# Performance work log

Measured on AMD Instinct MI355X. Metric: run time of the kernel, lower is better.

The kernel has to match this reference:

```python
import jax, jax.numpy as jnp
import numpy as np

B, T, G, D = 32, 120, 25, 256
H, HD = 8, 32  # H*HD == D
EPS = 1e-6


def _xavier(key, out_f, in_f):
    lim = float(np.sqrt(6.0 / (in_f + out_f)))
    return jax.random.uniform(key, (out_f, in_f), jnp.float32, -lim, lim)


def setup_inputs() -> dict:
    key = jax.random.key(0)
    ks = jax.random.split(key, 12)
    inp = {
        "x": jax.random.normal(ks[0], (B, T, G, D), jnp.float32),
        "adjacency_matrix": jax.random.uniform(ks[1], (G, G), jnp.float32),
        "Wq": _xavier(ks[2], H * HD, D), "bq": jnp.zeros((H * HD,), jnp.float32),
        "Wk": _xavier(ks[3], H * HD, D), "bk": jnp.zeros((H * HD,), jnp.float32),
        "Wv": _xavier(ks[4], H * HD, D), "bv": jnp.zeros((H * HD,), jnp.float32),
        "Wo": _xavier(ks[5], D, D), "bo": jnp.zeros((D,), jnp.float32),
        "Wfc": _xavier(ks[6], D, D), "bfc": jnp.zeros((D,), jnp.float32),
        "alpha": jnp.ones((D,), jnp.float32),
        "beta": jnp.zeros((D,), jnp.float32),
    }
    return inp


def _norm(z, alpha, beta):
    # torch: alpha * (x - mean) / (std(unbiased) + eps) + bias
    mu = jnp.mean(z, axis=-1, keepdims=True)
    sd = jnp.std(z, axis=-1, keepdims=True, ddof=1)
    return alpha * (z - mu) / (sd + EPS) + beta


def reference(x, adjacency_matrix, Wq, bq, Wk, bk, Wv, bv, Wo, bo, Wfc, bfc, alpha, beta):
    # adjacency aggregation: [G,G] @ [B,T,G,D] -> [B,T,G,D]
    h = jnp.einsum('gn,btnd->btgd', adjacency_matrix, x)

    def proj(W, b):
        # [B,T,G,D] -> [B,T,G,H,HD] -> transpose(1,2) -> [B,G,T,H,HD]
        p = (h @ W.T + b).reshape(B, T, G, H, HD)
        return jnp.swapaxes(p, 1, 2)

    Q, K, V = proj(Wq, bq), proj(Wk, bk), proj(Wv, bv)
    # scores over last two axes (H x H) -- faithful to the source's transpose quirk
    scores = (Q @ jnp.swapaxes(K, -2, -1)) / jnp.sqrt(jnp.float32(HD))  # [B,G,T,H,H]
    # F.softmax with no dim on a 5-D tensor -> torch softmaxes along dim=1 (G axis)
    w = jax.nn.softmax(scores, axis=1)
    att = w @ V  # [B,G,T,H,HD]
    att = jnp.swapaxes(att, 1, 2).reshape(B, T, G, D)
    x_att = att @ Wo.T + bo

    x1 = _norm(x + x_att, alpha, beta)
    x_fc = jax.nn.relu(x1 @ Wfc.T + bfc)
    return _norm(x1 + x_fc, alpha, beta)
```

## Files before the change

### kernel.cpp

```cpp
#include <hip/hip_runtime.h>

#define NB 32
#define NT 120
#define NG 25
#define ND 256
#define NH 8
#define NHD 32
#define NTH 512

typedef unsigned short u16;
typedef unsigned int u32;

typedef __bf16 bf16x8 __attribute__((ext_vector_type(8)));
typedef float  f32x4  __attribute__((ext_vector_type(4)));

#define SB 264
#define SF 268
#define OFF_HS_HI 0
#define OFF_HS_LO 16896
#define OFF_QKV   33792
#define OFF_ADJ   136704
#define OFF_SS    139312
#define OFF_WRED  145712
#define OFF_MU    146544
#define OFF_RSD   146656
#define SMEM_TOT  146768

#define WS_QKV_HI 0
#define WS_QKV_LO 196608
#define WS_WO_HI  393216
#define WS_WO_LO  458752
#define WS_WFC_HI 524288
#define WS_WFC_LO 589824
#define WS_NEED_BYTES (655360ull * 2ull)

__device__ __forceinline__ float bf2f(u16 u) { return __uint_as_float(((u32)u) << 16); }
__device__ __forceinline__ u16 f2bf(float f) {
    u32 x = __float_as_uint(f);
    return (u16)((x + 0x7FFFu + ((x >> 16) & 1u)) >> 16);
}
__device__ __forceinline__ void splitf(float v, u16& h, u16& l) {
    h = f2bf(v);
    l = f2bf(v - bf2f(h));
}
__device__ __forceinline__ bf16x8 ld_bf8(const u16* p) {
    uint4 u = *(const uint4*)p;
    return __builtin_bit_cast(bf16x8, u);
}

__global__ __launch_bounds__(256)
void prep_w(const float* __restrict__ Wq, const float* __restrict__ Wk,
            const float* __restrict__ Wv, const float* __restrict__ Wo,
            const float* __restrict__ Wfc, u16* __restrict__ ws) {
    int e = blockIdx.x * 256 + threadIdx.x;
    float v; int hi_base, lo_base, idx;
    if (e < 196608) {
        int n = e >> 8, k = e & 255;
        const float* W = (n < 256) ? Wq : (n < 512 ? Wk : Wv);
        v = W[(n & 255) * 256 + k];
        hi_base = WS_QKV_HI; lo_base = WS_QKV_LO; idx = e;
    } else if (e < 262144) {
        idx = e - 196608; v = Wo[idx];
        hi_base = WS_WO_HI; lo_base = WS_WO_LO;
    } else {
        idx = e - 262144; v = Wfc[idx];
        hi_base = WS_WFC_HI; lo_base = WS_WFC_LO;
    }
    u16 h, l; splitf(v, h, l);
    ws[hi_base + idx] = h;
    ws[lo_base + idx] = l;
}

__device__ __forceinline__ void norm_stats8(const float* zv, int gn,
                                            int lane, int wid, int tid,
                                            float (*s_wred)[13][2], float* s_mu, float* s_rsd) {
    #pragma unroll
    for (int i = 0; i < 13; ++i) {
        if (i >= gn) break;
        float s = zv[i], q = zv[i] * zv[i];
        #pragma unroll
        for (int off = 32; off > 0; off >>= 1) {
            s += __shfl_xor(s, off, 64);
            q += __shfl_xor(q, off, 64);
        }
        if (lane == 0) { s_wred[wid][i][0] = s; s_wred[wid][i][1] = q; }
    }
    __syncthreads();
    if (tid < NG) {
        const int g = tid;
        const int wb = (g < 13) ? 0 : 4, lg = (g < 13) ? g : g - 13;
        float s = 0.f, q = 0.f;
        #pragma unroll
        for (int w = 0; w < 4; ++w) { s += s_wred[wb + w][lg][0]; q += s_wred[wb + w][lg][1]; }
        float mu = s * (1.f / 256.f);
        float var = fmaxf((q - 256.f * mu * mu) * (1.f / 255.f), 0.f);
        s_mu[g] = mu;
        s_rsd[g] = 1.f / (sqrtf(var) + 1e-6f);
    }
    __syncthreads();
}

template<bool PREP>
__device__ __forceinline__ void load_bfrag(const u16* wshi, const u16* wslo,
                                           const float* Wf, int row, int koff,
                                           bf16x8& bh, bf16x8& bl) {
    if constexpr (PREP) {
        const int off = row * 256 + koff;
        bh = ld_bf8(wshi + off);
        bl = ld_bf8(wslo + off);
    } else {
        const float* p = Wf + row * 256 + koff;
        float4 w0 = *(const float4*)p, w1 = *(const float4*)(p + 4);
        float wv[8] = {w0.x, w0.y, w0.z, w0.w, w1.x, w1.y, w1.z, w1.w};
        union { u16 s[8]; bf16x8 v; } H, L;
        #pragma unroll
        for (int j = 0; j < 8; ++j) splitf(wv[j], H.s[j], L.s[j]);
        bh = H.v; bl = L.v;
    }
}

template<bool PREP>
__global__ __launch_bounds__(NTH, 2)
void enc_mfma(const float* __restrict__ x,  const float* __restrict__ adj,
              const float* __restrict__ Wq, const float* __restrict__ bq,
              const float* __restrict__ Wk, const float* __restrict__ bk,
              const float* __restrict__ Wv, const float* __restrict__ bv,
              const float* __restrict__ Wo, const float* __restrict__ bo,
              const float* __restrict__ Wfc,const float* __restrict__ bfc,
              const float* __restrict__ alpha, const float* __restrict__ beta,
              float* __restrict__ out, const u16* __restrict__ ws)
{
    extern __shared__ char smem[];
    u16*   hs_hi = (u16*)(smem + OFF_HS_HI);
    u16*   hs_lo = (u16*)(smem + OFF_HS_LO);
    float* qkvf  = (float*)(smem + OFF_QKV);
    float* adjf  = (float*)(smem + OFF_ADJ);
    float* ss    = (float*)(smem + OFF_SS);
    float (*s_wred)[13][2] = (float(*)[13][2])(smem + OFF_WRED);
    float* s_mu  = (float*)(smem + OFF_MU);
    float* s_rsd = (float*)(smem + OFF_RSD);

    const int bt = blockIdx.x;
    const int tid = threadIdx.x;
    const int d = tid & 255, rep = tid >> 8;
    const int lane = tid & 63, wid = tid >> 6;
    const int lm = lane & 15, quad = lane >> 4;
    const int g0 = rep ? 13 : 0, gn = rep ? 12 : 13;
    const long base = (long)bt * (NG * ND);

    auto loadA = [&](int k0, bf16x8 (&ah)[2], bf16x8 (&al)[2]) {
        const int koff = k0 + quad * 8;
        #pragma unroll
        for (int mt = 0; mt < 2; ++mt) {
            const int off = (mt * 16 + lm) * SB + koff;
            ah[mt] = ld_bf8(hs_hi + off);
            al[mt] = ld_bf8(hs_lo + off);
        }
    };
    auto loadB_qkv = [&](int k0, bf16x8 (&bh)[6], bf16x8 (&bl)[6]) {
        const int koff = k0 + quad * 8;
        #pragma unroll
        for (int j = 0; j < 6; ++j) {
            const int n0 = wid * 96 + j * 16;
            const int mat = n0 >> 8;
            const float* Wf = (mat == 0) ? Wq : (mat == 1 ? Wk : Wv);
            load_bfrag<PREP>(ws + WS_QKV_HI, ws + WS_QKV_LO, Wf,
                             PREP ? (n0 + lm) : ((n0 & 255) + lm), koff, bh[j], bl[j]);
        }
    };
    auto loadB_wo = [&](int k0, bf16x8 (&bh)[2], bf16x8 (&bl)[2]) {
        const int koff = k0 + quad * 8;
        #pragma unroll
        for (int j = 0; j < 2; ++j)
            load_bfrag<PREP>(ws + WS_WO_HI, ws + WS_WO_LO, Wo,
                             wid * 32 + j * 16 + lm, koff, bh[j], bl[j]);
    };
    auto loadB_wfc = [&](int k0, bf16x8 (&bh)[2], bf16x8 (&bl)[2]) {
        const int koff = k0 + quad * 8;
        #pragma unroll
        for (int j = 0; j < 2; ++j)
            load_bfrag<PREP>(ws + WS_WFC_HI, ws + WS_WFC_LO, Wfc,
                             wid * 32 + j * 16 + lm, koff, bh[j], bl[j]);
    };

    bf16x8 bh2[2][6], bl2[2][6];
    bf16x8 bh6[2][2], bl6[2][2];
    bf16x8 bh8[2][2], bl8[2][2];
    float zx[13];
    float zv[13];

    for (int i = tid; i < NG * NG; i += NTH) adjf[i] = adj[i];
    const float af = alpha[d], bef = beta[d];
    __syncthreads();

    {
        float acc[13];
        #pragma unroll
        for (int i = 0; i < 13; ++i) acc[i] = 0.f;
        #pragma unroll
        for (int n = 0; n < NG; ++n) {
            float xv = x[base + n * ND + d];
            if (rep == 0) { if (n < 13) zx[n] = xv; }
            else          { if (n >= 13) zx[n - 13] = xv; }
            #pragma unroll
            for (int i = 0; i < 13; ++i)
                acc[i] += adjf[(g0 + i) * NG + n] * xv;
        }
        #pragma unroll
        for (int i = 0; i < 13; ++i) {
            if (i >= gn) break;
            u16 h, l; splitf(acc[i], h, l);
            hs_hi[(g0 + i) * SB + d] = h; hs_lo[(g0 + i) * SB + d] = l;
        }
        if (rep) {
            #pragma unroll
            for (int g = NG; g < 32; ++g) { hs_hi[g * SB + d] = 0; hs_lo[g * SB + d] = 0; }
        }
    }
    loadB_qkv(0, bh2[0], bl2[0]);
    __syncthreads();

    {
        float bb[6];
        #pragma unroll
        for (int nt = 0; nt < 6; ++nt) {
            const int n0 = wid * 96 + nt * 16;
            const int mat = n0 >> 8, cb = (n0 & 255) + lm;
            const float* bp = (mat == 0) ? bq : (mat == 1 ? bk : bv);
            bb[nt] = bp[cb];
        }
        f32x4 acc[2][6];
        #pragma unroll
        for (int mt = 0; mt < 2; ++mt)
            #pragma unroll
            for (int nt = 0; nt < 6; ++nt) acc[mt][nt] = (f32x4)0.f;

        bf16x8 ah[2][2], al[2][2];
        loadA(0, ah[0], al[0]);
        #pragma unroll
        for (int ki = 0; ki < 8; ++ki) {
            const int cur = ki & 1, nxt = cur ^ 1;
            if (ki < 7) {
                loadB_qkv(32 * (ki + 1), bh2[nxt], bl2[nxt]);
                loadA(32 * (ki + 1), ah[nxt], al[nxt]);
            }
            #pragma unroll
            for (int j = 0; j < 6; ++j)
                #pragma unroll
                for (int mt = 0; mt < 2; ++mt)
                    acc[mt][j] = __builtin_amdgcn_mfma_f32_16x16x32_bf16(ah[cur][mt], bh2[cur][j], acc[mt][j], 0, 0, 0);
            #pragma unroll
            for (int j = 0; j < 6; ++j)
                #pragma unroll
                for (int mt = 0; mt < 2; ++mt)
                    acc[mt][j] = __builtin_amdgcn_mfma_f32_16x16x32_bf16(al[cur][mt], bh2[cur][j], acc[mt][j], 0, 0, 0);
            #pragma unroll
            for (int j = 0; j < 6; ++j)
                #pragma unroll
                for (int mt = 0; mt < 2; ++mt)
                    acc[mt][j] = __builtin_amdgcn_mfma_f32_16x16x32_bf16(ah[cur][mt], bl2[cur][j], acc[mt][j], 0, 0, 0);
        }
        #pragma unroll
        for (int nt = 0; nt < 6; ++nt) {
            const int n0 = wid * 96 + nt * 16;
            const int mat = n0 >> 8, cb = (n0 & 255) + lm;
            float* plane = qkvf + mat * (32 * SF);
            #pragma unroll
            for (int mt = 0; mt < 2; ++mt)
                #pragma unroll
                for (int i = 0; i < 4; ++i)
                    plane[(mt * 16 + quad * 4 + i) * SF + cb] = acc[mt][nt][i] + bb[nt];
        }
    }
    __syncthreads();

    for (int i = tid; i < NG * 64; i += NTH) {
        const int g = i >> 6, hh = i & 63;
        const float4* q4 = (const float4*)(qkvf + 0 * 32 * SF + g * SF + (hh >> 3) * NHD);
        const float4* k4 = (const float4*)(qkvf + 1 * 32 * SF + g * SF + (hh & 7) * NHD);
        float s = 0.f;
        #pragma unroll
        for (int c = 0; c < 8; ++c) {
            float4 qa = q4[c], ka = k4[c];
            s += qa.x * ka.x + qa.y * ka.y + qa.z * ka.z + qa.w * ka.w;
        }
        ss[i] = s * 0.17677669529663687f;
    }
    __syncthreads();

    {
        float* s_sm = adjf;
        const int col = tid & 63, part = tid >> 6;
        float m = -1e30f;
        for (int g = part; g < NG; g += 8) m = fmaxf(m, ss[g * 64 + col]);
        s_sm[part * 64 + col] = m;
        __syncthreads();
        float cm = -1e30f;
        #pragma unroll
        for (int p = 0; p < 8; ++p) cm = fmaxf(cm, s_sm[p * 64 + col]);
        __syncthreads();
        float den = 0.f;
        for (int g = part; g < NG; g += 8) {
            float e = expf(ss[g * 64 + col] - cm);
            ss[g * 64 + col] = e;
            den += e;
        }
        s_sm[part * 64 + col] = den;
        __syncthreads();
        float tden = 0.f;
        #pragma unroll
        for (int p = 0; p < 8; ++p) tden += s_sm[p * 64 + col];
        const float inv = 1.f / tden;
        for (int g = part; g < NG; g += 8) ss[g * 64 + col] *= inv;
    }
    __syncthreads();

    {
        const int h1 = (tid >> 5) & 7, hd = tid & 31;
        const float* Vp = qkvf + 2 * 32 * SF;
        #pragma unroll
        for (int i = 0; i < 13; ++i) {
            if (i >= gn) break;
            const int g = g0 + i;
            float a = 0.f;
            #pragma unroll
            for (int h2 = 0; h2 < NH; ++h2)
                a += ss[g * 64 + h1 * 8 + h2] * Vp[g * SF + h2 * NHD + hd];
            u16 h, l; splitf(a, h, l);
            hs_hi[g * SB + d] = h; hs_lo[g * SB + d] = l;
        }
    }
    loadB_wo(0, bh6[0], bl6[0]);
    __syncthreads();

    {
        float bb[2] = { bo[wid * 32 + lm], bo[wid * 32 + 16 + lm] };
        f32x4 acc[2][2];
        #pragma unroll
        for (int mt = 0; mt < 2; ++mt)
            #pragma unroll
            for (int nt = 0; nt < 2; ++nt) acc[mt][nt] = (f32x4)0.f;

        bf16x8 ah[2][2], al[2][2];
        loadA(0, ah[0], al[0]);
        #pragma unroll
        for (int ki = 0; ki < 8; ++ki) {
            const int cur = ki & 1, nxt = cur ^ 1;
            if (ki < 7) {
                loadB_wo(32 * (ki + 1), bh6[nxt], bl6[nxt]);
                loadA(32 * (ki + 1), ah[nxt], al[nxt]);
            }
            #pragma unroll
            for (int j = 0; j < 2; ++j)
                #pragma unroll
                for (int mt = 0; mt < 2; ++mt)
                    acc[mt][j] = __builtin_amdgcn_mfma_f32_16x16x32_bf16(ah[cur][mt], bh6[cur][j], acc[mt][j], 0, 0, 0);
            #pragma unroll
            for (int j = 0; j < 2; ++j)
                #pragma unroll
                for (int mt = 0; mt < 2; ++mt)
                    acc[mt][j] = __builtin_amdgcn_mfma_f32_16x16x32_bf16(al[cur][mt], bh6[cur][j], acc[mt][j], 0, 0, 0);
            #pragma unroll
            for (int j = 0; j < 2; ++j)
                #pragma unroll
                for (int mt = 0; mt < 2; ++mt)
                    acc[mt][j] = __builtin_amdgcn_mfma_f32_16x16x32_bf16(ah[cur][mt], bl6[cur][j], acc[mt][j], 0, 0, 0);
        }
        float* zs = qkvf;
        #pragma unroll
        for (int nt = 0; nt < 2; ++nt) {
            const int col = wid * 32 + nt * 16 + lm;
            #pragma unroll
            for (int mt = 0; mt < 2; ++mt)
                #pragma unroll
                for (int i = 0; i < 4; ++i)
                    zs[(mt * 16 + quad * 4 + i) * SF + col] = acc[mt][nt][i] + bb[nt];
        }
    }
    __syncthreads();

    {
        float* zs = qkvf;
        #pragma unroll
        for (int i = 0; i < 13; ++i) {
            if (i >= gn) break;
            zv[i] = zs[(g0 + i) * SF + d] + zx[i];
        }
    }
    norm_stats8(zv, gn, lane, wid, tid, s_wred, s_mu, s_rsd);
    #pragma unroll
    for (int i = 0; i < 13; ++i) {
        if (i >= gn) break;
        const float x1 = af * (zv[i] - s_mu[g0 + i]) * s_rsd[g0 + i] + bef;
        zv[i] = x1;
        u16 h, l; splitf(x1, h, l);
        hs_hi[(g0 + i) * SB + d] = h; hs_lo[(g0 + i) * SB + d] = l;
    }
    loadB_wfc(0, bh8[0], bl8[0]);
    __syncthreads();

    {
        float bb[2] = { bfc[wid * 32 + lm], bfc[wid * 32 + 16 + lm] };
        f32x4 acc[2][2];
        #pragma unroll
        for (int mt = 0; mt < 2; ++mt)
            #pragma unroll
            for (int nt = 0; nt < 2; ++nt) acc[mt][nt] = (f32x4)0.f;

        bf16x8 ah[2][2], al[2][2];
        loadA(0, ah[0], al[0]);
        #pragma unroll
        for (int ki = 0; ki < 8; ++ki) {
            const int cur = ki & 1, nxt = cur ^ 1;
            if (ki < 7) {
                loadB_wfc(32 * (ki + 1), bh8[nxt], bl8[nxt]);
                loadA(32 * (ki + 1), ah[nxt], al[nxt]);
            }
            #pragma unroll
            for (int j = 0; j < 2; ++j)
                #pragma unroll
                for (int mt = 0; mt < 2; ++mt)
                    acc[mt][j] = __builtin_amdgcn_mfma_f32_16x16x32_bf16(ah[cur][mt], bh8[cur][j], acc[mt][j], 0, 0, 0);
            #pragma unroll
            for (int j = 0; j < 2; ++j)
                #pragma unroll
                for (int mt = 0; mt < 2; ++mt)
                    acc[mt][j] = __builtin_amdgcn_mfma_f32_16x16x32_bf16(al[cur][mt], bh8[cur][j], acc[mt][j], 0, 0, 0);
            #pragma unroll
            for (int j = 0; j < 2; ++j)
                #pragma unroll
                for (int mt = 0; mt < 2; ++mt)
                    acc[mt][j] = __builtin_amdgcn_mfma_f32_16x16x32_bf16(ah[cur][mt], bl8[cur][j], acc[mt][j], 0, 0, 0);
        }
        float* zs = qkvf;
        #pragma unroll
        for (int nt = 0; nt < 2; ++nt) {
            const int col = wid * 32 + nt * 16 + lm;
            #pragma unroll
            for (int mt = 0; mt < 2; ++mt)
                #pragma unroll
                for (int i = 0; i < 4; ++i)
                    zs[(mt * 16 + quad * 4 + i) * SF + col] = fmaxf(acc[mt][nt][i] + bb[nt], 0.f);
        }
    }
    __syncthreads();

    float z2[13];
    {
        float* zs = qkvf;
        #pragma unroll
        for (int i = 0; i < 13; ++i) {
            if (i >= gn) break;
            z2[i] = zv[i] + zs[(g0 + i) * SF + d];
        }
    }
    norm_stats8(z2, gn, lane, wid, tid, s_wred, s_mu, s_rsd);
    #pragma unroll
    for (int i = 0; i < 13; ++i) {
        if (i >= gn) break;
        out[base + (g0 + i) * ND + d] = af * (z2[i] - s_mu[g0 + i]) * s_rsd[g0 + i] + bef;
    }
}

extern "C" void kernel_launch(void* const* d_in, const int* in_sizes, int n_in,
                              void* d_out, int out_size, void* d_ws, size_t ws_size,
                              hipStream_t stream) {
    (void)in_sizes; (void)n_in; (void)out_size;
    const float* x     = (const float*)d_in[0];
    const float* adj   = (const float*)d_in[1];
    const float* Wq    = (const float*)d_in[2];
    const float* bq    = (const float*)d_in[3];
    const float* Wk    = (const float*)d_in[4];
    const float* bk    = (const float*)d_in[5];
    const float* Wv    = (const float*)d_in[6];
    const float* bv    = (const float*)d_in[7];
    const float* Wo    = (const float*)d_in[8];
    const float* bo    = (const float*)d_in[9];
    const float* Wfc   = (const float*)d_in[10];
    const float* bfc   = (const float*)d_in[11];
    const float* alpha = (const float*)d_in[12];
    const float* beta  = (const float*)d_in[13];
    float* out = (float*)d_out;
    u16* ws = (u16*)d_ws;

    const bool prep = (ws_size >= WS_NEED_BYTES);

    hipFuncSetAttribute((const void*)enc_mfma<true>,
                        hipFuncAttributeMaxDynamicSharedMemorySize, SMEM_TOT);
    hipFuncSetAttribute((const void*)enc_mfma<false>,
                        hipFuncAttributeMaxDynamicSharedMemorySize, SMEM_TOT);

    if (prep) {
        prep_w<<<dim3(1280), dim3(256), 0, stream>>>(Wq, Wk, Wv, Wo, Wfc, ws);
        enc_mfma<true><<<dim3(NB * NT), dim3(NTH), SMEM_TOT, stream>>>(
            x, adj, Wq, bq, Wk, bk, Wv, bv, Wo, bo, Wfc, bfc, alpha, beta, out, ws);
    } else {
        enc_mfma<false><<<dim3(NB * NT), dim3(NTH), SMEM_TOT, stream>>>(
            x, adj, Wq, bq, Wk, bk, Wv, bv, Wo, bo, Wfc, bfc, alpha, beta, out, ws);
    }
}
```

Measured before the change: 991.2 us.

## Shrink LDS footprint by splitting V projection and reusing planes for higher occupancy

Splits the fused QKV projection into a QK pass followed by a separate V pass after softmax, so only two 25-row float planes are needed. Scores are kept in registers and Q/K columns are XOR-swizzled to avoid bank conflicts. Padded rows are zero-filled in registers instead of stored. LDS use drops from about 147KB to about 80KB and launch bounds rise to 4 blocks per CU, aiming at more concurrent blocks at the cost of tighter register limits and extra barriers.

```diff
diff --git a/kernel.cpp b/kernel.cpp
--- a/kernel.cpp
+++ b/kernel.cpp
@@ -15,16 +15,16 @@
 typedef float  f32x4  __attribute__((ext_vector_type(4)));
 
 #define SB 264
-#define SF 268
+#define SQ 260
 #define OFF_HS_HI 0
-#define OFF_HS_LO 16896
-#define OFF_QKV   33792
-#define OFF_ADJ   136704
-#define OFF_SS    139312
-#define OFF_WRED  145712
-#define OFF_MU    146544
-#define OFF_RSD   146656
-#define SMEM_TOT  146768
+#define OFF_HS_LO 13200
+#define OFF_P0    26400
+#define OFF_P1    52400
+#define OFF_SM    78400
+#define SMEM_TOT  80448
+#define OFF_WRED  26400
+#define OFF_MU    27232
+#define OFF_RSD   27344
 
 #define WS_QKV_HI 0
 #define WS_QKV_LO 196608
@@ -46,6 +46,10 @@
 __device__ __forceinline__ bf16x8 ld_bf8(const u16* p) {
     uint4 u = *(const uint4*)p;
     return __builtin_bit_cast(bf16x8, u);
+}
+__device__ __forceinline__ bf16x8 zero_bf8() {
+    uint4 z{0u, 0u, 0u, 0u};
+    return __builtin_bit_cast(bf16x8, z);
 }
 
 __global__ __launch_bounds__(256)
@@ -120,7 +124,7 @@
 }
 
 template<bool PREP>
-__global__ __launch_bounds__(NTH, 2)
+__global__ __launch_bounds__(NTH, 4)
 void enc_mfma(const float* __restrict__ x,  const float* __restrict__ adj,
               const float* __restrict__ Wq, const float* __restrict__ bq,
               const float* __restrict__ Wk, const float* __restrict__ bk,
@@ -131,11 +135,11 @@
               float* __restrict__ out, const u16* __restrict__ ws)
 {
     extern __shared__ char smem[];
-    u16*   hs_hi = (u16*)(smem + OFF_HS_HI);
-    u16*   hs_lo = (u16*)(smem + OFF_HS_LO);
-    float* qkvf  = (float*)(smem + OFF_QKV);
-    float* adjf  = (float*)(smem + OFF_ADJ);
-    float* ss    = (float*)(smem + OFF_SS);
+    u16*   hs_hi  = (u16*)(smem + OFF_HS_HI);
+    u16*   hs_lo  = (u16*)(smem + OFF_HS_LO);
+    float* plane0 = (float*)(smem + OFF_P0);
+    float* plane1 = (float*)(smem + OFF_P1);
+    float* s_sm   = (float*)(smem + OFF_SM);
     float (*s_wred)[13][2] = (float(*)[13][2])(smem + OFF_WRED);
     float* s_mu  = (float*)(smem + OFF_MU);
     float* s_rsd = (float*)(smem + OFF_RSD);
@@ -150,22 +154,34 @@
 
     auto loadA = [&](int k0, bf16x8 (&ah)[2], bf16x8 (&al)[2]) {
         const int koff = k0 + quad * 8;
-        #pragma unroll
-        for (int mt = 0; mt < 2; ++mt) {
-            const int off = (mt * 16 + lm) * SB + koff;
-            ah[mt] = ld_bf8(hs_hi + off);
-            al[mt] = ld_bf8(hs_lo + off);
+        ah[0] = ld_bf8(hs_hi + lm * SB + koff);
+        al[0] = ld_bf8(hs_lo + lm * SB + koff);
+        if (lm < 9) {
+            ah[1] = ld_bf8(hs_hi + (16 + lm) * SB + koff);
+            al[1] = ld_bf8(hs_lo + (16 + lm) * SB + koff);
+        } else {
+            ah[1] = zero_bf8();
+            al[1] = zero_bf8();
         }
     };
-    auto loadB_qkv = [&](int k0, bf16x8 (&bh)[6], bf16x8 (&bl)[6]) {
+    auto loadB_qk = [&](int k0, bf16x8 (&bh)[4], bf16x8 (&bl)[4]) {
         const int koff = k0 + quad * 8;
         #pragma unroll
-        for (int j = 0; j < 6; ++j) {
-            const int n0 = wid * 96 + j * 16;
+        for (int j = 0; j < 4; ++j) {
+            const int n0 = wid * 64 + j * 16;
             const int mat = n0 >> 8;
-            const float* Wf = (mat == 0) ? Wq : (mat == 1 ? Wk : Wv);
+            const float* Wf = (mat == 0) ? Wq : Wk;
             load_bfrag<PREP>(ws + WS_QKV_HI, ws + WS_QKV_LO, Wf,
                              PREP ? (n0 + lm) : ((n0 & 255) + lm), koff, bh[j], bl[j]);
+        }
+    };
+    auto loadB_v = [&](int k0, bf16x8 (&bh)[2], bf16x8 (&bl)[2]) {
+        const int koff = k0 + quad * 8;
+        #pragma unroll
+        for (int j = 0; j < 2; ++j) {
+            const int n0 = wid * 32 + j * 16;
+            load_bfrag<PREP>(ws + WS_QKV_HI, ws + WS_QKV_LO, Wv,
+                             PREP ? (512 + n0 + lm) : (n0 + lm), koff, bh[j], bl[j]);
         }
     };
     auto loadB_wo = [&](int k0, bf16x8 (&bh)[2], bf16x8 (&bl)[2]) {
@@ -183,13 +199,14 @@
                              wid * 32 + j * 16 + lm, koff, bh[j], bl[j]);
     };
 
-    bf16x8 bh2[2][6], bl2[2][6];
-    bf16x8 bh6[2][2], bl6[2][2];
-    bf16x8 bh8[2][2], bl8[2][2];
+    bf16x8 bhQK[2][4], blQK[2][4];
+    bf16x8 bhV[2][2],  blV[2][2];
+    bf16x8 bh6[2][2],  bl6[2][2];
+    bf16x8 bh8[2][2],  bl8[2][2];
     float zx[13];
     float zv[13];
 
-    for (int i = tid; i < NG * NG; i += NTH) adjf[i] = adj[i];
+    for (int i = tid; i < NG * NG; i += NTH) plane0[i] = adj[i];
     const float af = alpha[d], bef = beta[d];
     __syncthreads();
 
@@ -204,7 +221,7 @@
             else          { if (n >= 13) zx[n - 13] = xv; }
             #pragma unroll
             for (int i = 0; i < 13; ++i)
-                acc[i] += adjf[(g0 + i) * NG + n] * xv;
+                acc[i] += plane0[(g0 + i) * NG + n] * xv;
         }
         #pragma unroll
         for (int i = 0; i < 13; ++i) {
@@ -212,28 +229,23 @@
             u16 h, l; splitf(acc[i], h, l);
             hs_hi[(g0 + i) * SB + d] = h; hs_lo[(g0 + i) * SB + d] = l;
         }
-        if (rep) {
-            #pragma unroll
-            for (int g = NG; g < 32; ++g) { hs_hi[g * SB + d] = 0; hs_lo[g * SB + d] = 0; }
-        }
-    }
-    loadB_qkv(0, bh2[0], bl2[0]);
-    __syncthreads();
-
-    {
-        float bb[6];
-        #pragma unroll
-        for (int nt = 0; nt < 6; ++nt) {
-            const int n0 = wid * 96 + nt * 16;
+    }
+    loadB_qk(0, bhQK[0], blQK[0]);
+    __syncthreads();
+
+    {
+        float bb[4];
+        #pragma unroll
+        for (int nt = 0; nt < 4; ++nt) {
+            const int n0 = wid * 64 + nt * 16;
             const int mat = n0 >> 8, cb = (n0 & 255) + lm;
-            const float* bp = (mat == 0) ? bq : (mat == 1 ? bk : bv);
-            bb[nt] = bp[cb];
-        }
-        f32x4 acc[2][6];
+            bb[nt] = (mat ? bk : bq)[cb];
+        }
+        f32x4 acc[2][4];
         #pragma unroll
         for (int mt = 0; mt < 2; ++mt)
             #pragma unroll
-            for (int nt = 0; nt < 6; ++nt) acc[mt][nt] = (f32x4)0.f;
+            for (int nt = 0; nt < 4; ++nt) acc[mt][nt] = (f32x4)0.f;
 
         bf16x8 ah[2][2], al[2][2];
         loadA(0, ah[0], al[0]);
@@ -241,58 +253,70 @@
         for (int ki = 0; ki < 8; ++ki) {
             const int cur = ki & 1, nxt = cur ^ 1;
             if (ki < 7) {
-                loadB_qkv(32 * (ki + 1), bh2[nxt], bl2[nxt]);
+                loadB_qk(32 * (ki + 1), bhQK[nxt], blQK[nxt]);
                 loadA(32 * (ki + 1), ah[nxt], al[nxt]);
             }
             #pragma unroll
-            for (int j = 0; j < 6; ++j)
-                #pragma unroll
-                for (int mt = 0; mt < 2; ++mt)
-                    acc[mt][j] = __builtin_amdgcn_mfma_f32_16x16x32_bf16(ah[cur][mt], bh2[cur][j], acc[mt][j], 0, 0, 0);
-            #pragma unroll
-            for (int j = 0; j < 6; ++j)
-                #pragma unroll
-                for (int mt = 0; mt < 2; ++mt)
-                    acc[mt][j] = __builtin_amdgcn_mfma_f32_16x16x32_bf16(al[cur][mt], bh2[cur][j], acc[mt][j], 0, 0, 0);
-            #pragma unroll
-            for (int j = 0; j < 6; ++j)
-                #pragma unroll
-                for (int mt = 0; mt < 2; ++mt)
-                    acc[mt][j] = __builtin_amdgcn_mfma_f32_16x16x32_bf16(ah[cur][mt], bl2[cur][j], acc[mt][j], 0, 0, 0);
-        }
-        #pragma unroll
-        for (int nt = 0; nt < 6; ++nt) {
-            const int n0 = wid * 96 + nt * 16;
-            const int mat = n0 >> 8, cb = (n0 & 255) + lm;
-            float* plane = qkvf + mat * (32 * SF);
+            for (int j = 0; j < 4; ++j)
+                #pragma unroll
+                for (int mt = 0; mt < 2; ++mt)
+                    acc[mt][j] = __builtin_amdgcn_mfma_f32_16x16x32_bf16(ah[cur][mt], bhQK[cur][j], acc[mt][j], 0, 0, 0);
+            #pragma unroll
+            for (int j = 0; j < 4; ++j)
+                #pragma unroll
+                for (int mt = 0; mt < 2; ++mt)
+                    acc[mt][j] = __builtin_amdgcn_mfma_f32_16x16x32_bf16(al[cur][mt], bhQK[cur][j], acc[mt][j], 0, 0, 0);
+            #pragma unroll
+            for (int j = 0; j < 4; ++j)
+                #pragma unroll
+                for (int mt = 0; mt < 2; ++mt)
+                    acc[mt][j] = __builtin_amdgcn_mfma_f32_16x16x32_bf16(ah[cur][mt], blQK[cur][j], acc[mt][j], 0, 0, 0);
+        }
+        #pragma unroll
+        for (int nt = 0; nt < 4; ++nt) {
+            const int n0 = wid * 64 + nt * 16;
+            const int mat = n0 >> 8, col = (n0 & 255) + lm;
+            const int pcol = col ^ ((col >> 3) & 0x1C);
+            float* plane = mat ? plane1 : plane0;
             #pragma unroll
             for (int mt = 0; mt < 2; ++mt)
                 #pragma unroll
-                for (int i = 0; i < 4; ++i)
-                    plane[(mt * 16 + quad * 4 + i) * SF + cb] = acc[mt][nt][i] + bb[nt];
-        }
-    }
-    __syncthreads();
-
-    for (int i = tid; i < NG * 64; i += NTH) {
-        const int g = i >> 6, hh = i & 63;
-        const float4* q4 = (const float4*)(qkvf + 0 * 32 * SF + g * SF + (hh >> 3) * NHD);
-        const float4* k4 = (const float4*)(qkvf + 1 * 32 * SF + g * SF + (hh & 7) * NHD);
-        float s = 0.f;
-        #pragma unroll
-        for (int c = 0; c < 8; ++c) {
-            float4 qa = q4[c], ka = k4[c];
-            s += qa.x * ka.x + qa.y * ka.y + qa.z * ka.z + qa.w * ka.w;
-        }
-        ss[i] = s * 0.17677669529663687f;
-    }
-    __syncthreads();
-
-    {
-        float* s_sm = adjf;
+                for (int i = 0; i < 4; ++i) {
+                    const int r = mt * 16 + quad * 4 + i;
+                    if (mt == 0 || r < 25)
+                        plane[r * SQ + pcol] = acc[mt][nt][i] + bb[nt];
+                }
+        }
+    }
+    __syncthreads();
+
+    float sreg[4];
+    {
+        #pragma unroll
+        for (int kk = 0; kk < 4; ++kk) {
+            const int i = tid + kk * NTH;
+            const int ii = (i < NG * 64) ? i : 0;
+            const int g = ii >> 6, hh = ii & 63;
+            const int jq = hh >> 3, jk = hh & 7;
+            const float4* q4 = (const float4*)(plane0 + g * SQ + jq * 32);
+            const float4* k4 = (const float4*)(plane1 + g * SQ + jk * 32);
+            float s = 0.f;
+            #pragma unroll
+            for (int c = 0; c < 8; ++c) {
+                float4 qa = q4[c ^ jq], ka = k4[c ^ jk];
+                s += qa.x * ka.x + qa.y * ka.y + qa.z * ka.z + qa.w * ka.w;
+            }
+            sreg[kk] = s * 0.17677669529663687f;
+        }
+    }
+    __syncthreads();
+
+    {
         const int col = tid & 63, part = tid >> 6;
         float m = -1e30f;
-        for (int g = part; g < NG; g += 8) m = fmaxf(m, ss[g * 64 + col]);
+        #pragma unroll
+        for (int kk = 0; kk < 4; ++kk)
+            if (tid + kk * NTH < NG * 64) m = fmaxf(m, sreg[kk]);
         s_sm[part * 64 + col] = m;
         __syncthreads();
         float cm = -1e30f;
@@ -300,24 +324,78 @@
         for (int p = 0; p < 8; ++p) cm = fmaxf(cm, s_sm[p * 64 + col]);
         __syncthreads();
         float den = 0.f;
-        for (int g = part; g < NG; g += 8) {
-            float e = expf(ss[g * 64 + col] - cm);
-            ss[g * 64 + col] = e;
-            den += e;
-        }
+        #pragma unroll
+        for (int kk = 0; kk < 4; ++kk)
+            if (tid + kk * NTH < NG * 64) {
+                float e = expf(sreg[kk] - cm);
+                sreg[kk] = e;
+                den += e;
+            }
         s_sm[part * 64 + col] = den;
         __syncthreads();
         float tden = 0.f;
         #pragma unroll
         for (int p = 0; p < 8; ++p) tden += s_sm[p * 64 + col];
         const float inv = 1.f / tden;
-        for (int g = part; g < NG; g += 8) ss[g * 64 + col] *= inv;
+        #pragma unroll
+        for (int kk = 0; kk < 4; ++kk) {
+            const int i = tid + kk * NTH;
+            if (i < NG * 64) plane1[i] = sreg[kk] * inv;
+        }
+    }
+    loadB_v(0, bhV[0], blV[0]);
+    __syncthreads();
+
+    {
+        float bb[2] = { bv[wid * 32 + lm], bv[wid * 32 + 16 + lm] };
+        f32x4 acc[2][2];
+        #pragma unroll
+        for (int mt = 0; mt < 2; ++mt)
+            #pragma unroll
+            for (int nt = 0; nt < 2; ++nt) acc[mt][nt] = (f32x4)0.f;
+
+        bf16x8 ah[2][2], al[2][2];
+        loadA(0, ah[0], al[0]);
+        #pragma unroll
+        for (int ki = 0; ki < 8; ++ki) {
+            const int cur = ki & 1, nxt = cur ^ 1;
+            if (ki < 7) {
+                loadB_v(32 * (ki + 1), bhV[nxt], blV[nxt]);
+                loadA(32 * (ki + 1), ah[nxt], al[nxt]);
+            }
+            #pragma unroll
+            for (int j = 0; j < 2; ++j)
+                #pragma unroll
+                for (int mt = 0; mt < 2; ++mt)
+                    acc[mt][j] = __builtin_amdgcn_mfma_f32_16x16x32_bf16(ah[cur][mt], bhV[cur][j], acc[mt][j], 0, 0, 0);
+            #pragma unroll
+            for (int j = 0; j < 2; ++j)
+                #pragma unroll
+                for (int mt = 0; mt < 2; ++mt)
+                    acc[mt][j] = __builtin_amdgcn_mfma_f32_16x16x32_bf16(al[cur][mt], bhV[cur][j], acc[mt][j], 0, 0, 0);
+            #pragma unroll
+            for (int j = 0; j < 2; ++j)
+                #pragma unroll
+                for (int mt = 0; mt < 2; ++mt)
+                    acc[mt][j] = __builtin_amdgcn_mfma_f32_16x16x32_bf16(ah[cur][mt], blV[cur][j], acc[mt][j], 0, 0, 0);
+        }
+        #pragma unroll
+        for (int nt = 0; nt < 2; ++nt) {
+            const int col = wid * 32 + nt * 16 + lm;
+            #pragma unroll
+            for (int mt = 0; mt < 2; ++mt)
+                #pragma unroll
+                for (int i = 0; i < 4; ++i) {
+                    const int r = mt * 16 + quad * 4 + i;
+                    if (mt == 0 || r < 25)
+                        plane0[r * SQ + col] = acc[mt][nt][i] + bb[nt];
+                }
+        }
     }
     __syncthreads();
 
     {
         const int h1 = (tid >> 5) & 7, hd = tid & 31;
-        const float* Vp = qkvf + 2 * 32 * SF;
         #pragma unroll
         for (int i = 0; i < 13; ++i) {
             if (i >= gn) break;
@@ -325,7 +403,7 @@
             float a = 0.f;
             #pragma unroll
             for (int h2 = 0; h2 < NH; ++h2)
-                a += ss[g * 64 + h1 * 8 + h2] * Vp[g * SF + h2 * NHD + hd];
+                a += plane1[g * 64 + h1 * 8 + h2] * plane0[g * SQ + h2 * NHD + hd];
             u16 h, l; splitf(a, h, l);
             hs_hi[g * SB + d] = h; hs_lo[g * SB + d] = l;
         }
@@ -366,25 +444,26 @@
                 for (int mt = 0; mt < 2; ++mt)
                     acc[mt][j] = __builtin_amdgcn_mfma_f32_16x16x32_bf16(ah[cur][mt], bl6[cur][j], acc[mt][j], 0, 0, 0);
         }
-        float* zs = qkvf;
         #pragma unroll
         for (int nt = 0; nt < 2; ++nt) {
             const int col = wid * 32 + nt * 16 + lm;
             #pragma unroll
             for (int mt = 0; mt < 2; ++mt)
                 #pragma unroll
-                for (int i = 0; i < 4; ++i)
-                    zs[(mt * 16 + quad * 4 + i) * SF + col] = acc[mt][nt][i] + bb[nt];
-        }
-    }
-    __syncthreads();
-
-    {
-        float* zs = qkvf;
+                for (int i = 0; i < 4; ++i) {
+                    const int r = mt * 16 + quad * 4 + i;
+                    if (mt == 0 || r < 25)
+                        plane1[r * SQ + col] = acc[mt][nt][i] + bb[nt];
+                }
+        }
+    }
+    __syncthreads();
+
+    {
         #pragma unroll
         for (int i = 0; i < 13; ++i) {
             if (i >= gn) break;
-            zv[i] = zs[(g0 + i) * SF + d] + zx[i];
+            zv[i] = plane1[(g0 + i) * SQ + d] + zx[i];
         }
     }
     norm_stats8(zv, gn, lane, wid, tid, s_wred, s_mu, s_rsd);
@@ -432,26 +511,27 @@
                 for (int mt = 0; mt < 2; ++mt)
                     acc[mt][j] = __builtin_amdgcn_mfma_f32_16x16x32_bf16(ah[cur][mt], bl8[cur][j], acc[mt][j], 0, 0, 0);
         }
-        float* zs = qkvf;
         #pragma unroll
         for (int nt = 0; nt < 2; ++nt) {
             const int col = wid * 32 + nt * 16 + lm;
             #pragma unroll
             for (int mt = 0; mt < 2; ++mt)
                 #pragma unroll
-                for (int i = 0; i < 4; ++i)
-                    zs[(mt * 16 + quad * 4 + i) * SF + col] = fmaxf(acc[mt][nt][i] + bb[nt], 0.f);
+                for (int i = 0; i < 4; ++i) {
+                    const int r = mt * 16 + quad * 4 + i;
+                    if (mt == 0 || r < 25)
+                        plane1[r * SQ + col] = fmaxf(acc[mt][nt][i] + bb[nt], 0.f);
+                }
         }
     }
     __syncthreads();
 
     float z2[13];
     {
-        float* zs = qkvf;
         #pragma unroll
         for (int i = 0; i < 13; ++i) {
             if (i >= gn) break;
-            z2[i] = zv[i] + zs[(g0 + i) * SF + d];
+            z2[i] = zv[i] + plane1[(g0 + i) * SQ + d];
         }
     }
     norm_stats8(z2, gn, lane, wid, tid, s_wred, s_mu, s_rsd);
```

Measured after the change: 1.997 ms. +101.5%, slower.
